# Performance work log

Hardware: AMD Instinct MI355X
Metric: run time of the kernel (lower is better)

The kernel has to match this reference:

```python
import jax, jax.numpy as jnp
import numpy as np

N = 100000   # nodes
DEG = 16     # in-degree per node
E = N * DEG  # edges
D = 64       # embedding_dim


def mobius_addition(x, y, c):
    xy = jnp.sum(x * y, axis=-1, keepdims=True)
    x2 = jnp.sum(x * x, axis=-1, keepdims=True)
    y2 = jnp.sum(y * y, axis=-1, keepdims=True)
    num = (1 + 2 * c * xy + c * y2) * x + (1 - c * x2) * y
    den = 1 + 2 * c * xy + c * c * x2 * y2
    return num / den


def exp_map(x, v, c):
    vn = jnp.linalg.norm(v, axis=-1, keepdims=True)
    sc = jnp.sqrt(c)
    second = jnp.tanh(sc * vn / 2) * v / (sc * vn)
    return mobius_addition(x, second, c)


def log_map(x, y, c):
    add = mobius_addition(-x, y, c)
    an = jnp.linalg.norm(add, axis=-1, keepdims=True)
    sc = jnp.sqrt(c)
    return 2 / sc * jnp.arctanh(sc * an) * add / an


def setup_inputs() -> dict:
    key = jax.random.key(0)
    ks = jax.random.split(key, 6)
    # scale so points are well inside the Poincare ball (atanh domain)
    x = jax.random.normal(ks[0], (N, D), jnp.float32) * 0.01
    src = jax.random.randint(ks[1], (E,), 0, N, dtype=jnp.int32)
    # every node gets exactly DEG in-edges -> no isolated nodes (avoids 0/0 in exp_map)
    dst = jnp.repeat(jnp.arange(N, dtype=jnp.int32), DEG)
    s = 1.0 / np.sqrt(D)
    Wq = jax.random.normal(ks[2], (D, D), jnp.float32) * s
    Wk = jax.random.normal(ks[3], (D, D), jnp.float32) * s
    Wv = jax.random.normal(ks[4], (D, D), jnp.float32) * s
    bq = jnp.zeros((D,), jnp.float32)
    bk = jnp.zeros((D,), jnp.float32)
    bv = jnp.zeros((D,), jnp.float32)
    curvature = jnp.ones((1,), jnp.float32)
    return {"x": x, "curvature": curvature, "Wq": Wq, "bq": bq, "Wk": Wk,
            "bk": bk, "Wv": Wv, "bv": bv, "src": src, "dst": dst}


def reference(x, curvature, Wq, bq, Wk, bk, Wv, bv, src, dst):
    c = curvature  # (1,), broadcasts against (N,1) keepdim norms
    n = x.shape[0]
    origin = jnp.zeros_like(x[:1])  # (1, D)
    tangent = log_map(origin, x, c)  # (N, D)
    # torch nn.Linear: y = x @ W.T + b
    q = tangent @ Wq.T + bq
    k = tangent @ Wk.T + bk
    v = tangent @ Wv.T + bv
    scale = jnp.asarray(x.shape[-1] ** 0.5, x.dtype)
    # per-edge score: <k[src], q[dst]> / sqrt(d)
    scores = jnp.einsum('ed,ed->e', k[src], q[dst]) / scale  # (E,)
    # segment (per-dst) softmax over incoming edges
    smax = jax.ops.segment_max(scores, dst, num_segments=n)
    ex = jnp.exp(scores - smax[dst])
    ssum = jax.ops.segment_sum(ex, dst, num_segments=n)
    alpha = ex / ssum[dst]  # (E,)
    # weighted scatter-sum of src values
    h = jax.ops.segment_sum(alpha[:, None] * v[src], dst, num_segments=n)  # (N, D)
    return exp_map(origin, h, c)
```

## Files before the change

### kernel.cpp

```cpp
#include <hip/hip_runtime.h>
#include <hip/hip_bf16.h>
#include <math.h>


typedef __attribute__((ext_vector_type(8))) short bf16x8;
typedef __attribute__((ext_vector_type(4))) float f32x4;
typedef __attribute__((ext_vector_type(2))) float f32x2;

static __device__ __forceinline__ short f2bf(float f) {
    union { __hip_bfloat16 h; short s; } u; u.h = __float2bfloat16(f); return u.s;
}
static __device__ __forceinline__ float bflo(unsigned u) {
    return __uint_as_float(u << 16);
}
static __device__ __forceinline__ float bfhi(unsigned u) {
    return __uint_as_float(u & 0xffff0000u);
}

#define TSTRIDE 72
#define SQSTR   72
#define SKSTR   72
#define SVSTR   68

__global__ __launch_bounds__(256) void qkv_kernel(
    const float* __restrict__ x,
    const float* __restrict__ cur,
    const float* __restrict__ Wq, const float* __restrict__ bq,
    const float* __restrict__ Wk, const float* __restrict__ bk,
    const float* __restrict__ Wv, const float* __restrict__ bv,
    unsigned short* __restrict__ qb, unsigned char* __restrict__ kvl,
    float* __restrict__ vs, int N)
{
    __shared__ short tL[128 * TSTRIDE];
    __shared__ short sq[16 * SQSTR];
    __shared__ unsigned char sk[16 * SKSTR];
    __shared__ float svf[16 * SVSTR];
    const int tid = threadIdx.x;
    const int w = tid >> 6, lane = tid & 63;
    const int blockBase = blockIdx.x * 128;
    const float sc = sqrtf(cur[0]);

    const int rr = lane >> 2, p = lane & 3;
    #pragma unroll
    for (int it = 0; it < 2; ++it) {
        const int rloc = w * 32 + it * 16 + rr;
        int row = blockBase + rloc; if (row >= N) row = N - 1;
        const float4* xr = (const float4*)(x + (size_t)row * 64 + p * 16);
        float4 x0 = xr[0], x1 = xr[1], x2 = xr[2], x3 = xr[3];
        float pn = x0.x*x0.x + x0.y*x0.y + x0.z*x0.z + x0.w*x0.w
                 + x1.x*x1.x + x1.y*x1.y + x1.z*x1.z + x1.w*x1.w
                 + x2.x*x2.x + x2.y*x2.y + x2.z*x2.z + x2.w*x2.w
                 + x3.x*x3.x + x3.y*x3.y + x3.z*x3.z + x3.w*x3.w;
        pn += __shfl_xor(pn, 1, 64);
        pn += __shfl_xor(pn, 2, 64);
        float z = sc * sqrtf(pn);
        float ts = (z > 1e-12f) ? (__logf((1.0f + z) / (1.0f - z)) / z) : 2.0f;
        bf16x8 t0, t1;
        t0[0]=f2bf(ts*x0.x); t0[1]=f2bf(ts*x0.y); t0[2]=f2bf(ts*x0.z); t0[3]=f2bf(ts*x0.w);
        t0[4]=f2bf(ts*x1.x); t0[5]=f2bf(ts*x1.y); t0[6]=f2bf(ts*x1.z); t0[7]=f2bf(ts*x1.w);
        t1[0]=f2bf(ts*x2.x); t1[1]=f2bf(ts*x2.y); t1[2]=f2bf(ts*x2.z); t1[3]=f2bf(ts*x2.w);
        t1[4]=f2bf(ts*x3.x); t1[5]=f2bf(ts*x3.y); t1[6]=f2bf(ts*x3.z); t1[7]=f2bf(ts*x3.w);
        bf16x8* dst = (bf16x8*)&tL[rloc * TSTRIDE + p * 16];
        dst[0] = t0; dst[1] = t1;
    }
    __syncthreads();

    const int n16 = lane & 15, quad = lane >> 4;
    bf16x8 Bf[3][2];
    float bias[3];
    int matv[3], col0v[3];
    #pragma unroll
    for (int tt = 0; tt < 3; ++tt) {
        const int tile = w * 3 + tt;
        const int mat = tile >> 2;
        const int col0 = (tile & 3) * 16;
        matv[tt] = mat; col0v[tt] = col0;
        const float* Wm = (mat == 0) ? Wq : (mat == 1) ? Wk : Wv;
        const float* bm = (mat == 0) ? bq : (mat == 1) ? bk : bv;
        const float* srcp = Wm + (col0 + n16) * 64 + quad * 8;
        #pragma unroll
        for (int h = 0; h < 2; ++h) {
            float4 a = *(const float4*)(srcp + h * 32);
            float4 b = *(const float4*)(srcp + h * 32 + 4);
            bf16x8 f;
            f[0]=f2bf(a.x); f[1]=f2bf(a.y); f[2]=f2bf(a.z); f[3]=f2bf(a.w);
            f[4]=f2bf(b.x); f[5]=f2bf(b.y); f[6]=f2bf(b.z); f[7]=f2bf(b.w);
            Bf[tt][h] = f;
        }
        bias[tt] = bm[col0 + n16];
    }

    const int crow = tid >> 4;
    const int c8   = tid & 15;

    for (int nt = 0; nt < 8; ++nt) {
        const short* ar = &tL[(nt * 16 + n16) * TSTRIDE + quad * 8];
        bf16x8 A0 = *(const bf16x8*)ar;
        bf16x8 A1 = *(const bf16x8*)(ar + 32);
        #pragma unroll
        for (int tt = 0; tt < 3; ++tt) {
            f32x4 acc = { bias[tt], bias[tt], bias[tt], bias[tt] };
            acc = __builtin_amdgcn_mfma_f32_16x16x32_bf16(A0, Bf[tt][0], acc, 0, 0, 0);
            acc = __builtin_amdgcn_mfma_f32_16x16x32_bf16(A1, Bf[tt][1], acc, 0, 0, 0);
            const int mat = matv[tt], col0 = col0v[tt];
            #pragma unroll
            for (int r4 = 0; r4 < 4; ++r4) {
                const int rl = quad * 4 + r4;
                const int c  = col0 + n16;
                if (mat == 0) {
                    sq[rl * SQSTR + c] = f2bf(acc[r4]);
                } else if (mat == 1) {
                    int pk = __builtin_amdgcn_cvt_pk_fp8_f32(acc[r4], acc[r4], 0, false);
                    sk[rl * SKSTR + c] = (unsigned char)(pk & 0xff);
                } else {
                    svf[rl * SVSTR + c] = acc[r4];
                }
            }
        }
        __syncthreads();

        const int node = blockBase + nt * 16 + crow;
        {
            f32x4 v4 = *(const f32x4*)&svf[crow * SVSTR + c8 * 4];
            float m = fmaxf(fmaxf(fabsf(v4[0]), fabsf(v4[1])),
                            fmaxf(fabsf(v4[2]), fabsf(v4[3])));
            m = fmaxf(m, __shfl_xor(m, 1, 64));
            m = fmaxf(m, __shfl_xor(m, 2, 64));
            m = fmaxf(m, __shfl_xor(m, 4, 64));
            m = fmaxf(m, __shfl_xor(m, 8, 64));
            float rm = fmaxf(m, 1e-20f);
            float inv = 127.0f / rm;
            float scale = rm * (1.0f / 127.0f);
            int i0 = __float2int_rn(v4[0] * inv);
            int i1 = __float2int_rn(v4[1] * inv);
            int i2 = __float2int_rn(v4[2] * inv);
            int i3 = __float2int_rn(v4[3] * inv);
            unsigned pk = (unsigned)(i0 & 255) | ((unsigned)(i1 & 255) << 8)
                        | ((unsigned)(i2 & 255) << 16) | ((unsigned)(i3 & 255) << 24);
            if (node < N) {
                *(uint2*)(qb + (size_t)node * 64 + c8 * 4) =
                    *(const uint2*)&sq[crow * SQSTR + c8 * 4];
                *(unsigned*)(kvl + (size_t)node * 128 + c8 * 4) =
                    *(const unsigned*)&sk[crow * SKSTR + c8 * 4];
                *(unsigned*)(kvl + (size_t)node * 128 + 64 + c8 * 4) = pk;
                if (c8 == 0) vs[node] = scale;
            }
        }
        __syncthreads();
    }
}

__global__ __launch_bounds__(256) void attn_kernel(
    const unsigned short* __restrict__ qb, const unsigned char* __restrict__ kvl,
    const float* __restrict__ vs, const int* __restrict__ src,
    const float* __restrict__ cur,
    float* __restrict__ out, int N)
{
    const int tid = threadIdx.x;
    const int w = tid >> 6, lane = tid & 63;
    int node = blockIdx.x * 4 + w;
    if (node >= N) node = N - 1;

    const int j = lane >> 2, p = lane & 3;
    const int sj = src[node * 16 + j];

    const int half = lane >> 5, l5 = lane & 31;
    const int sbase = 32 * half;
    int srcv[8];
    #pragma unroll
    for (int i = 0; i < 8; ++i) srcv[i] = __shfl(sj, sbase + 4 * i, 64);
    unsigned short vraw[8];
    #pragma unroll
    for (int i = 0; i < 8; ++i)
        vraw[i] = *(const unsigned short*)(kvl + (size_t)srcv[i] * 128 + 64 + (l5 << 1));

    uint4 kd = *(const uint4*)(kvl + (size_t)sj * 128 + p * 16);
    const uint4* qp = (const uint4*)(qb + (size_t)node * 64 + p * 16);
    uint4 qa = qp[0], qc = qp[1];
    const float sjs = vs[sj];
    float acc = 0.f;
    {
        f32x2 k0 = __builtin_amdgcn_cvt_pk_f32_fp8(kd.x, false);
        f32x2 k1 = __builtin_amdgcn_cvt_pk_f32_fp8(kd.x, true);
        acc = fmaf(k0[0], bflo(qa.x), acc); acc = fmaf(k0[1], bfhi(qa.x), acc);
        acc = fmaf(k1[0], bflo(qa.y), acc); acc = fmaf(k1[1], bfhi(qa.y), acc);
        k0 = __builtin_amdgcn_cvt_pk_f32_fp8(kd.y, false);
        k1 = __builtin_amdgcn_cvt_pk_f32_fp8(kd.y, true);
        acc = fmaf(k0[0], bflo(qa.z), acc); acc = fmaf(k0[1], bfhi(qa.z), acc);
        acc = fmaf(k1[0], bflo(qa.w), acc); acc = fmaf(k1[1], bfhi(qa.w), acc);
        k0 = __builtin_amdgcn_cvt_pk_f32_fp8(kd.z, false);
        k1 = __builtin_amdgcn_cvt_pk_f32_fp8(kd.z, true);
        acc = fmaf(k0[0], bflo(qc.x), acc); acc = fmaf(k0[1], bfhi(qc.x), acc);
        acc = fmaf(k1[0], bflo(qc.y), acc); acc = fmaf(k1[1], bfhi(qc.y), acc);
        k0 = __builtin_amdgcn_cvt_pk_f32_fp8(kd.w, false);
        k1 = __builtin_amdgcn_cvt_pk_f32_fp8(kd.w, true);
        acc = fmaf(k0[0], bflo(qc.z), acc); acc = fmaf(k0[1], bfhi(qc.z), acc);
        acc = fmaf(k1[0], bflo(qc.w), acc); acc = fmaf(k1[1], bfhi(qc.w), acc);
    }
    acc += __shfl_xor(acc, 1, 64);
    acc += __shfl_xor(acc, 2, 64);
    float score = acc * 0.125f;

    float ex = __expf(score);
    float ssum = ex;
    #pragma unroll
    for (int m = 4; m < 64; m <<= 1) ssum += __shfl_xor(ssum, m, 64);
    float myas = (ex / ssum) * sjs;

    float asv[8];
    #pragma unroll
    for (int i = 0; i < 8; ++i) asv[i] = __shfl(myas, sbase + 4 * i, 64);
    float hx = 0.f, hy = 0.f;
    #pragma unroll
    for (int i = 0; i < 8; ++i) {
        int u = (int)vraw[i];
        float flo = (float)((u << 24) >> 24);
        float fhi = (float)((short)u >> 8);
        hx = fmaf(asv[i], flo, hx);
        hy = fmaf(asv[i], fhi, hy);
    }
    hx += __shfl_xor(hx, 32, 64);
    hy += __shfl_xor(hy, 32, 64);

    float n2 = hx * hx + hy * hy;
    #pragma unroll
    for (int m = 1; m < 32; m <<= 1) n2 += __shfl_xor(n2, m, 64);
    const float sc = sqrtf(cur[0]);
    float z = sc * sqrtf(n2);
    float e = __expf(z);
    float scale = (z > 1e-12f) ? ((e - 1.0f) / (z * (e + 1.0f))) : 0.5f;
    if (half == 0) {
        float2 o2 = make_float2(scale * hx, scale * hy);
        *(float2*)(out + (size_t)node * 64 + (l5 << 1)) = o2;
    }
}

extern "C" void kernel_launch(void* const* d_in, const int* in_sizes, int n_in,
                              void* d_out, int out_size, void* d_ws, size_t ws_size,
                              hipStream_t stream)
{
    const float* x   = (const float*)d_in[0];
    const float* cur = (const float*)d_in[1];
    const float* Wq  = (const float*)d_in[2];
    const float* bq  = (const float*)d_in[3];
    const float* Wk  = (const float*)d_in[4];
    const float* bk  = (const float*)d_in[5];
    const float* Wv  = (const float*)d_in[6];
    const float* bv  = (const float*)d_in[7];
    const int* src = (const int*)d_in[8];

    const int N = in_sizes[0] / 64;

    unsigned short* qb  = (unsigned short*)d_ws;
    unsigned char*  kvl = (unsigned char*)(qb + (size_t)N * 64);
    float*          vsc = (float*)(kvl + (size_t)N * 128);

    const int blocks1 = (N + 127) / 128;
    const int blocks2 = (N + 3) / 4;
    qkv_kernel<<<blocks1, 256, 0, stream>>>(x, cur, Wq, bq, Wk, bk, Wv, bv,
                                            qb, kvl, vsc, N);
    attn_kernel<<<blocks2, 256, 0, stream>>>(qb, kvl, vsc, src, cur,
                                             (float*)d_out, N);
}
```

Measured before the change: 150.5 us.

## Precompute weight fragments in prep kernel and store Q as fp32 directly

Adds a single-block prep kernel that converts Wq/Wk/Wv to bf16 MFMA fragments and biases once, so each qkv block loads ready-made fragments instead of converting weights itself. Q is now written as fp32 straight from the MFMA accumulators with scattered per-element stores, replacing the bf16 LDS staging and coalesced copy. The attention kernel then reads Q as fp32. This doubles the Q traffic and makes the Q writes uncoalesced, and adds an extra kernel launch, in exchange for less per-block conversion work and simpler dot-product arithmetic.

```diff
diff --git a/kernel.cpp b/kernel.cpp
--- a/kernel.cpp
+++ b/kernel.cpp
@@ -10,29 +10,49 @@
 static __device__ __forceinline__ short f2bf(float f) {
     union { __hip_bfloat16 h; short s; } u; u.h = __float2bfloat16(f); return u.s;
 }
-static __device__ __forceinline__ float bflo(unsigned u) {
-    return __uint_as_float(u << 16);
-}
-static __device__ __forceinline__ float bfhi(unsigned u) {
-    return __uint_as_float(u & 0xffff0000u);
-}
 
 #define TSTRIDE 72
-#define SQSTR   72
 #define SKSTR   72
 #define SVSTR   68
+
+__global__ __launch_bounds__(256) void prep_kernel(
+    const float* __restrict__ Wq, const float* __restrict__ bq,
+    const float* __restrict__ Wk, const float* __restrict__ bk,
+    const float* __restrict__ Wv, const float* __restrict__ bv,
+    short* __restrict__ wfrag, float* __restrict__ wbias)
+{
+    const int tid = threadIdx.x;
+    const int w = tid >> 6, lane = tid & 63;
+    const int n16 = lane & 15, quad = lane >> 4;
+    #pragma unroll
+    for (int tt = 0; tt < 3; ++tt) {
+        const int tile = w * 3 + tt;
+        const int mat = tile >> 2;
+        const int col0 = (tile & 3) * 16;
+        const float* Wm = (mat == 0) ? Wq : (mat == 1) ? Wk : Wv;
+        const float* bm = (mat == 0) ? bq : (mat == 1) ? bk : bv;
+        const float* srcp = Wm + (col0 + n16) * 64 + quad * 8;
+        #pragma unroll
+        for (int h = 0; h < 2; ++h) {
+            float4 a = *(const float4*)(srcp + h * 32);
+            float4 b = *(const float4*)(srcp + h * 32 + 4);
+            bf16x8 f;
+            f[0]=f2bf(a.x); f[1]=f2bf(a.y); f[2]=f2bf(a.z); f[3]=f2bf(a.w);
+            f[4]=f2bf(b.x); f[5]=f2bf(b.y); f[6]=f2bf(b.z); f[7]=f2bf(b.w);
+            *(bf16x8*)&wfrag[((tile * 64 + lane) * 2 + h) * 8] = f;
+        }
+        wbias[tile * 64 + lane] = bm[col0 + n16];
+    }
+}
 
 __global__ __launch_bounds__(256) void qkv_kernel(
     const float* __restrict__ x,
     const float* __restrict__ cur,
-    const float* __restrict__ Wq, const float* __restrict__ bq,
-    const float* __restrict__ Wk, const float* __restrict__ bk,
-    const float* __restrict__ Wv, const float* __restrict__ bv,
-    unsigned short* __restrict__ qb, unsigned char* __restrict__ kvl,
+    const short* __restrict__ wfrag, const float* __restrict__ wbias,
+    float* __restrict__ qf, unsigned char* __restrict__ kvl,
     float* __restrict__ vs, int N)
 {
     __shared__ short tL[128 * TSTRIDE];
-    __shared__ short sq[16 * SQSTR];
     __shared__ unsigned char sk[16 * SKSTR];
     __shared__ float svf[16 * SVSTR];
     const int tid = threadIdx.x;
@@ -72,22 +92,12 @@
     #pragma unroll
     for (int tt = 0; tt < 3; ++tt) {
         const int tile = w * 3 + tt;
-        const int mat = tile >> 2;
-        const int col0 = (tile & 3) * 16;
-        matv[tt] = mat; col0v[tt] = col0;
-        const float* Wm = (mat == 0) ? Wq : (mat == 1) ? Wk : Wv;
-        const float* bm = (mat == 0) ? bq : (mat == 1) ? bk : bv;
-        const float* srcp = Wm + (col0 + n16) * 64 + quad * 8;
-        #pragma unroll
-        for (int h = 0; h < 2; ++h) {
-            float4 a = *(const float4*)(srcp + h * 32);
-            float4 b = *(const float4*)(srcp + h * 32 + 4);
-            bf16x8 f;
-            f[0]=f2bf(a.x); f[1]=f2bf(a.y); f[2]=f2bf(a.z); f[3]=f2bf(a.w);
-            f[4]=f2bf(b.x); f[5]=f2bf(b.y); f[6]=f2bf(b.z); f[7]=f2bf(b.w);
-            Bf[tt][h] = f;
-        }
-        bias[tt] = bm[col0 + n16];
+        matv[tt] = tile >> 2;
+        col0v[tt] = (tile & 3) * 16;
+        const short* fp = &wfrag[((tile * 64 + lane) * 2) * 8];
+        Bf[tt][0] = *(const bf16x8*)fp;
+        Bf[tt][1] = *(const bf16x8*)(fp + 8);
+        bias[tt] = wbias[tile * 64 + lane];
     }
 
     const int crow = tid >> 4;
@@ -108,7 +118,8 @@
                 const int rl = quad * 4 + r4;
                 const int c  = col0 + n16;
                 if (mat == 0) {
-                    sq[rl * SQSTR + c] = f2bf(acc[r4]);
+                    const int node = blockBase + nt * 16 + rl;
+                    if (node < N) qf[(size_t)node * 64 + c] = acc[r4];
                 } else if (mat == 1) {
                     int pk = __builtin_amdgcn_cvt_pk_fp8_f32(acc[r4], acc[r4], 0, false);
                     sk[rl * SKSTR + c] = (unsigned char)(pk & 0xff);
@@ -138,8 +149,6 @@
             unsigned pk = (unsigned)(i0 & 255) | ((unsigned)(i1 & 255) << 8)
                         | ((unsigned)(i2 & 255) << 16) | ((unsigned)(i3 & 255) << 24);
             if (node < N) {
-                *(uint2*)(qb + (size_t)node * 64 + c8 * 4) =
-                    *(const uint2*)&sq[crow * SQSTR + c8 * 4];
                 *(unsigned*)(kvl + (size_t)node * 128 + c8 * 4) =
                     *(const unsigned*)&sk[crow * SKSTR + c8 * 4];
                 *(unsigned*)(kvl + (size_t)node * 128 + 64 + c8 * 4) = pk;
@@ -151,7 +160,7 @@
 }
 
 __global__ __launch_bounds__(256) void attn_kernel(
-    const unsigned short* __restrict__ qb, const unsigned char* __restrict__ kvl,
+    const float* __restrict__ qf, const unsigned char* __restrict__ kvl,
     const float* __restrict__ vs, const int* __restrict__ src,
     const float* __restrict__ cur,
     float* __restrict__ out, int N)
@@ -175,27 +184,27 @@
         vraw[i] = *(const unsigned short*)(kvl + (size_t)srcv[i] * 128 + 64 + (l5 << 1));
 
     uint4 kd = *(const uint4*)(kvl + (size_t)sj * 128 + p * 16);
-    const uint4* qp = (const uint4*)(qb + (size_t)node * 64 + p * 16);
-    uint4 qa = qp[0], qc = qp[1];
+    const float4* qr = (const float4*)(qf + (size_t)node * 64 + p * 16);
+    float4 q0 = qr[0], q1 = qr[1], q2 = qr[2], q3 = qr[3];
     const float sjs = vs[sj];
     float acc = 0.f;
     {
         f32x2 k0 = __builtin_amdgcn_cvt_pk_f32_fp8(kd.x, false);
         f32x2 k1 = __builtin_amdgcn_cvt_pk_f32_fp8(kd.x, true);
-        acc = fmaf(k0[0], bflo(qa.x), acc); acc = fmaf(k0[1], bfhi(qa.x), acc);
-        acc = fmaf(k1[0], bflo(qa.y), acc); acc = fmaf(k1[1], bfhi(qa.y), acc);
+        acc = fmaf(k0[0], q0.x, acc); acc = fmaf(k0[1], q0.y, acc);
+        acc = fmaf(k1[0], q0.z, acc); acc = fmaf(k1[1], q0.w, acc);
         k0 = __builtin_amdgcn_cvt_pk_f32_fp8(kd.y, false);
         k1 = __builtin_amdgcn_cvt_pk_f32_fp8(kd.y, true);
-        acc = fmaf(k0[0], bflo(qa.z), acc); acc = fmaf(k0[1], bfhi(qa.z), acc);
-        acc = fmaf(k1[0], bflo(qa.w), acc); acc = fmaf(k1[1], bfhi(qa.w), acc);
+        acc = fmaf(k0[0], q1.x, acc); acc = fmaf(k0[1], q1.y, acc);
+        acc = fmaf(k1[0], q1.z, acc); acc = fmaf(k1[1], q1.w, acc);
         k0 = __builtin_amdgcn_cvt_pk_f32_fp8(kd.z, false);
         k1 = __builtin_amdgcn_cvt_pk_f32_fp8(kd.z, true);
-        acc = fmaf(k0[0], bflo(qc.x), acc); acc = fmaf(k0[1], bfhi(qc.x), acc);
-        acc = fmaf(k1[0], bflo(qc.y), acc); acc = fmaf(k1[1], bfhi(qc.y), acc);
+        acc = fmaf(k0[0], q2.x, acc); acc = fmaf(k0[1], q2.y, acc);
+        acc = fmaf(k1[0], q2.z, acc); acc = fmaf(k1[1], q2.w, acc);
         k0 = __builtin_amdgcn_cvt_pk_f32_fp8(kd.w, false);
         k1 = __builtin_amdgcn_cvt_pk_f32_fp8(kd.w, true);
-        acc = fmaf(k0[0], bflo(qc.z), acc); acc = fmaf(k0[1], bfhi(qc.z), acc);
-        acc = fmaf(k1[0], bflo(qc.w), acc); acc = fmaf(k1[1], bfhi(qc.w), acc);
+        acc = fmaf(k0[0], q3.x, acc); acc = fmaf(k0[1], q3.y, acc);
+        acc = fmaf(k1[0], q3.z, acc); acc = fmaf(k1[1], q3.w, acc);
     }
     acc += __shfl_xor(acc, 1, 64);
     acc += __shfl_xor(acc, 2, 64);
@@ -251,14 +260,16 @@
 
     const int N = in_sizes[0] / 64;
 
-    unsigned short* qb  = (unsigned short*)d_ws;
-    unsigned char*  kvl = (unsigned char*)(qb + (size_t)N * 64);
+    float*          qf  = (float*)d_ws;
+    unsigned char*  kvl = (unsigned char*)(qf + (size_t)N * 64);
     float*          vsc = (float*)(kvl + (size_t)N * 128);
+    short*          wfr = (short*)(vsc + N);
+    float*          wbi = (float*)(wfr + 12 * 64 * 16);
 
     const int blocks1 = (N + 127) / 128;
     const int blocks2 = (N + 3) / 4;
-    qkv_kernel<<<blocks1, 256, 0, stream>>>(x, cur, Wq, bq, Wk, bk, Wv, bv,
-                                            qb, kvl, vsc, N);
-    attn_kernel<<<blocks2, 256, 0, stream>>>(qb, kvl, vsc, src, cur,
+    prep_kernel<<<1, 256, 0, stream>>>(Wq, bq, Wk, bk, Wv, bv, wfr, wbi);
+    qkv_kernel<<<blocks1, 256, 0, stream>>>(x, cur, wfr, wbi, qf, kvl, vsc, N);
+    attn_kernel<<<blocks2, 256, 0, stream>>>(qf, kvl, vsc, src, cur,
                                              (float*)d_out, N);
 }
```

Measured after the change: 153.6 us. +2.1%, slower.
